# Kernel tuning notes

Hardware: AMD Instinct MI355X
Metric: run time of the kernel (lower is better)

The kernel has to match this reference:

```python
import jax, jax.numpy as jnp
import numpy as np

B, C, BINS, W, FF, NB = 8, 16, 1024, 512, 2048, 4
EPS = 1e-5
DN = ('NCH', 'OIH', 'NCH')  # conv1d dimension numbers


def setup_inputs() -> dict:
    key = jax.random.key(0)
    ks = iter(jax.random.split(key, 40))
    def w(shape, fan_in):
        return jax.random.normal(next(ks), shape, jnp.float32) / np.float32(np.sqrt(fan_in))
    inp = {}
    inp['x'] = jax.random.normal(next(ks), (B, C, BINS, W), jnp.float32)
    inp['bl_w'] = w((C, 1), C)                     # bottleneck linear
    inp['bn_w'] = jnp.ones((1,), jnp.float32)
    inp['bn_b'] = jnp.zeros((1,), jnp.float32)
    inp['glu_w'] = w((BINS, 2 * BINS), BINS)
    inp['ln1_w'] = jnp.ones((BINS,), jnp.float32); inp['ln1_b'] = jnp.zeros((BINS,), jnp.float32)
    inp['c1L_w'] = w((BINS, 2 * FF), BINS)
    inp['c1R_w'] = w((FF // 2, BINS, 3), BINS * 3)  # OIW conv weight
    inp['ln2_w'] = jnp.ones((2 * FF,), jnp.float32); inp['ln2_b'] = jnp.zeros((2 * FF,), jnp.float32)
    inp['c2d_w'] = w((2 * FF, 1, 9), 9)             # depthwise conv, groups=2*FF
    inp['c2p_w'] = w((FF // 2, 2 * FF, 1), 2 * FF)  # pointwise conv
    inp['ln3_w'] = jnp.ones((BINS,), jnp.float32); inp['ln3_b'] = jnp.zeros((BINS,), jnp.float32)
    inp['q_w'] = w((BINS, BINS), BINS)
    inp['k_w'] = w((BINS, BINS), BINS)
    inp['v_w'] = w((BINS, BINS), BINS)
    inp['o_w'] = w((BINS, BINS), BINS)
    inp['er'] = w((BINS // NB, W), BINS // NB)      # relative-position embedding
    inp['dist_w'] = w((NB, W, 1), W)                # distance weight per band
    inp['ln4_w'] = jnp.ones((BINS,), jnp.float32); inp['ln4_b'] = jnp.zeros((BINS,), jnp.float32)
    inp['c3_w'] = w((BINS, 2 * FF), BINS)
    inp['c4_w'] = w((2 * FF, BINS), 2 * FF)
    inp['ln5_w'] = jnp.ones((BINS,), jnp.float32); inp['ln5_b'] = jnp.zeros((BINS,), jnp.float32)
    return inp


def _ln(x, w, b):
    m = jnp.mean(x, -1, keepdims=True)
    v = jnp.mean((x - m) ** 2, -1, keepdims=True)
    return (x - m) * jax.lax.rsqrt(v + EPS) * w + b


def _forward(x, bl_w, bn_w, bn_b, glu_w, ln1_w, ln1_b, c1L_w, c1R_w, ln2_w, ln2_b,
             c2d_w, c2p_w, ln3_w, ln3_b, q_w, k_w, v_w, o_w, er, dist_w,
             ln4_w, ln4_b, c3_w, c4_w, ln5_w, ln5_b):
    # bottleneck: channels -> 1, BatchNorm2d (training-mode batch stats), ReLU
    y = jnp.einsum('bchw,co->bohw', x, bl_w)          # [B,1,BINS,W]
    m = jnp.mean(y, axis=(0, 2, 3), keepdims=True)
    v = jnp.mean((y - m) ** 2, axis=(0, 2, 3), keepdims=True)
    y = jax.nn.relu((y - m) * jax.lax.rsqrt(v + EPS) * bn_w.reshape(1, -1, 1, 1)
                    + bn_b.reshape(1, -1, 1, 1))
    xt = y[:, 0].transpose(0, 2, 1)                   # [B,W,BINS]

    # GLU branch + residual + LN
    g = xt @ glu_w
    a_, b_ = jnp.split(g, 2, axis=-1)
    xt = _ln(xt + a_ * jax.nn.sigmoid(b_), ln1_w, ln1_b)

    # dual branch: linear (wide) + conv1d (narrow, zero-padded up)
    hL = jax.nn.relu(xt @ c1L_w)                      # [B,W,2*FF]
    hR = jax.lax.conv_general_dilated(xt.transpose(0, 2, 1), c1R_w, (1,), ((1, 1),),
                                      dimension_numbers=DN).transpose(0, 2, 1)
    hR = jax.nn.relu(hR)                              # [B,W,FF//2]
    h = _ln(hL + jnp.pad(hR, ((0, 0), (0, 0), (0, 2 * FF - FF // 2))), ln2_w, ln2_b)

    # depthwise conv (k=9) + pointwise conv
    hc = jax.lax.conv_general_dilated(h.transpose(0, 2, 1), c2d_w, (1,), ((4, 4),),
                                      dimension_numbers=DN, feature_group_count=2 * FF)
    hc = jax.lax.conv_general_dilated(hc, c2p_w, (1,), ((0, 0),), dimension_numbers=DN)
    h = hc.transpose(0, 2, 1)                         # [B,W,FF//2]
    xt = _ln(xt + jnp.pad(h, ((0, 0), (0, 0), (0, BINS - FF // 2))), ln3_w, ln3_b)

    # multiband frame attention with relative-position bias
    d = BINS // NB
    q = (xt @ q_w).reshape(B, W, NB, d).transpose(0, 2, 1, 3)   # [B,NB,W,d]
    k = (xt @ k_w).reshape(B, W, NB, d).transpose(0, 2, 1, 3)
    vv = (xt @ v_w).reshape(B, W, NB, d).transpose(0, 2, 1, 3)
    qk = jnp.einsum('bnid,bnjd->bnij', q, k) / np.float32(np.sqrt(BINS))
    qe = jnp.einsum('bnid,dj->bnij', q, er)                      # [B,NB,W,W]
    skew = jnp.pad(qe, ((0, 0), (0, 0), (0, 0), (1, 0))).swapaxes(2, 3)[:, :, 1:, :]
    idx = jnp.arange(W)
    dist = jnp.abs(idx[:, None] - idx[None, :]).astype(jnp.float32) / 2.0  # [W,W]
    p = dist[None] * dist_w + skew                               # [B,NB,W,W]
    a = jax.nn.softmax(qk + p, axis=-1)
    o = jnp.einsum('bnij,bnjd->bnid', a, vv).transpose(0, 2, 1, 3).reshape(B, W, BINS) @ o_w
    xt = _ln(xt + o, ln4_w, ln4_b)

    # FFN
    h = jax.nn.relu(xt @ c3_w) @ c4_w
    xt = _ln(xt + h, ln5_w, ln5_b)
    return xt.transpose(0, 2, 1)[:, None]             # [B,1,BINS,W]


def reference(x, bl_w, bn_w, bn_b, glu_w, ln1_w, ln1_b, c1L_w, c1R_w, ln2_w, ln2_b,
              c2d_w, c2p_w, ln3_w, ln3_b, q_w, k_w, v_w, o_w, er, dist_w,
              ln4_w, ln4_b, c3_w, c4_w, ln5_w, ln5_b):
    return _forward(x, bl_w, bn_w, bn_b, glu_w, ln1_w, ln1_b, c1L_w, c1R_w, ln2_w, ln2_b,
                    c2d_w, c2p_w, ln3_w, ln3_b, q_w, k_w, v_w, o_w, er, dist_w,
                    ln4_w, ln4_b, c3_w, c4_w, ln5_w, ln5_b)
```

## Files before the change

kernel.cpp:

```cpp
#include <hip/hip_runtime.h>
#include <stdint.h>

typedef unsigned short u16;
typedef __bf16 bf16x8_t __attribute__((ext_vector_type(8)));
typedef float f32x4_t __attribute__((ext_vector_type(4)));
typedef u16 u16x8 __attribute__((ext_vector_type(8)));

#define DEVINL static __device__ __forceinline__

DEVINL float b2f(u16 h){ union{unsigned u; float f;} v; v.u=((unsigned)h)<<16; return v.f; }
DEVINL u16 f2b(float f){ union{float f; unsigned u;} v; v.f=f; unsigned u=v.u; u += 0x7fffu + ((u>>16)&1u); return (u16)(u>>16); }

DEVINL void gload16(const void* g, void* lds){
  __builtin_amdgcn_global_load_lds((__attribute__((address_space(1))) void*)(void*)g,
                                   (__attribute__((address_space(3))) void*)lds, 16, 0, 0);
}

DEVINL void blk_sum2(float& a, float& b, float* sm){
  #pragma unroll
  for (int o=32;o;o>>=1){ a += __shfl_down(a,o,64); b += __shfl_down(b,o,64); }
  int tid = threadIdx.x;
  if ((tid&63)==0){ sm[(tid>>6)*2]=a; sm[(tid>>6)*2+1]=b; }
  __syncthreads();
  a = sm[0]+sm[2]+sm[4]+sm[6];
  b = sm[1]+sm[3]+sm[5]+sm[7];
  __syncthreads();
}

template<int EPI>
__global__ __launch_bounds__(256) void gemm_k(
    const u16* __restrict__ A, int lda, long aS1, long aS2,
    const u16* __restrict__ B, int ldb, long bS1, long bS2,
    void* __restrict__ Cv, int ldc, long cS1, long cS2,
    int K, int zdiv)
{
  __shared__ u16 sA[128*32];
  __shared__ u16 sB[128*32];
  const int tid = threadIdx.x;
  const int w = tid >> 6, l = tid & 63;
  const int z = blockIdx.z; const int z1 = z / zdiv, z2 = z % zdiv;
  const u16* Ab = A + z1*aS1 + z2*aS2;
  const u16* Bb = B + z1*bS1 + z2*bS2;
  const int rowB = blockIdx.y * 128, colB = blockIdx.x * 128;

  const int sr = w*32 + (l>>2);
  const int so = (l&3)*8;
  const u16* gA0 = Ab + (long)(rowB + sr)*lda + so;
  const u16* gA1 = gA0 + (long)16*lda;
  const u16* gB0 = Bb + (long)(colB + sr)*ldb + so;
  const u16* gB1 = gB0 + (long)16*ldb;
  u16* lA0 = sA + w*1024; u16* lA1 = lA0 + 512;
  u16* lB0 = sB + w*1024; u16* lB1 = lB0 + 512;

  const int lrow = l & 15, lg = l >> 4;
  const int wrow = w & 1, wcol = w >> 1;

  f32x4_t zz = {0.f,0.f,0.f,0.f};
  f32x4_t acc[4][4];
  #pragma unroll
  for (int mi=0; mi<4; ++mi)
    #pragma unroll
    for (int ni=0; ni<4; ++ni) acc[mi][ni] = zz;

  for (int k0 = 0; k0 < K; k0 += 32) {
    __syncthreads();
    gload16(gA0 + k0, lA0);
    gload16(gA1 + k0, lA1);
    gload16(gB0 + k0, lB0);
    gload16(gB1 + k0, lB1);
    __syncthreads();
    bf16x8_t af[4], bfr[4];
    #pragma unroll
    for (int mi=0; mi<4; ++mi)
      af[mi] = *(const bf16x8_t*)&sA[(wrow*64 + mi*16 + lrow)*32 + lg*8];
    #pragma unroll
    for (int ni=0; ni<4; ++ni)
      bfr[ni] = *(const bf16x8_t*)&sB[(wcol*64 + ni*16 + lrow)*32 + lg*8];
    #pragma unroll
    for (int mi=0; mi<4; ++mi)
      #pragma unroll
      for (int ni=0; ni<4; ++ni)
        acc[mi][ni] = __builtin_amdgcn_mfma_f32_16x16x32_bf16(af[mi], bfr[ni], acc[mi][ni], 0,0,0);
  }

  const long cb = z1*cS1 + z2*cS2;
  #pragma unroll
  for (int mi=0; mi<4; ++mi)
  #pragma unroll
  for (int ni=0; ni<4; ++ni)
  #pragma unroll
  for (int j=0; j<4; ++j) {
    const long rr = rowB + wrow*64 + mi*16 + lg*4 + j;
    const long cc = colB + wcol*64 + ni*16 + lrow;
    float v = acc[mi][ni][j];
    if (EPI == 2) ((float*)Cv)[cb + rr*(long)ldc + cc] = v;
    else {
      if (EPI == 1) v = fmaxf(v, 0.f);
      ((u16*)Cv)[cb + rr*(long)ldc + cc] = f2b(v);
    }
  }
}

__global__ __launch_bounds__(256) void k_tcvt(const float* __restrict__ src, u16* __restrict__ dst, int R, int Cc){
  __shared__ float s[32][33];
  int c0 = blockIdx.x*32, r0 = blockIdx.y*32;
  int tx = threadIdx.x, ty = threadIdx.y;
  #pragma unroll
  for (int k=0;k<4;++k)
    s[ty+8*k][tx] = src[(long)(r0+ty+8*k)*Cc + c0+tx];
  __syncthreads();
  #pragma unroll
  for (int k=0;k<4;++k)
    dst[(long)(c0+ty+8*k)*R + r0+tx] = f2b(s[tx][ty+8*k]);
}

__global__ __launch_bounds__(256) void k_cvt(const float* __restrict__ src, u16* __restrict__ dst){
  long base = (long)blockIdx.x*1024 + threadIdx.x;
  #pragma unroll
  for (int j=0;j<4;++j) dst[base + j*256] = f2b(src[base + j*256]);
}

__global__ __launch_bounds__(256) void k_c1rp(const float* __restrict__ src, u16* __restrict__ dst){
  int o = blockIdx.x; int kk = blockIdx.y*256 + threadIdx.x;
  int i = kk & 1023, t = kk >> 10;
  dst[(long)o*3072 + kk] = f2b(src[(long)o*3072 + i*3 + t]);
}

__global__ __launch_bounds__(256) void k_cdt(const float* __restrict__ src, float* __restrict__ dst){
  int idx = blockIdx.x*256 + threadIdx.x;
  int t = idx >> 12, f = idx & 4095;
  dst[idx] = src[f*9 + t];
}

__global__ void k_zero(float* p){ if (threadIdx.x < 2) p[threadIdx.x] = 0.f; }

__global__ __launch_bounds__(256) void k_bneck1(const float* __restrict__ x, const float* __restrict__ blw,
                                                float* __restrict__ X, float* __restrict__ stats){
  __shared__ float s[64][65];
  __shared__ float red[8];
  int b = blockIdx.z, h0 = blockIdx.y*64, w0 = blockIdx.x*64;
  int tid = threadIdx.x;
  int wl = tid & 63, hl = tid >> 6;
  float yacc[16];
  #pragma unroll
  for (int r=0;r<16;++r) yacc[r]=0.f;
  for (int c=0;c<16;++c){
    float wc = blw[c];
    const float* xp = x + (((long)(b*16 + c)*1024 + h0)*512 + w0);
    #pragma unroll
    for (int r=0;r<16;++r)
      yacc[r] += xp[(hl + 4*r)*512 + wl] * wc;
  }
  float s1=0.f, s2=0.f;
  #pragma unroll
  for (int r=0;r<16;++r){ s1+=yacc[r]; s2+=yacc[r]*yacc[r]; }
  #pragma unroll
  for (int o=32;o;o>>=1){ s1+=__shfl_down(s1,o,64); s2+=__shfl_down(s2,o,64); }
  if ((tid&63)==0){ red[(tid>>6)*2]=s1; red[(tid>>6)*2+1]=s2; }
  #pragma unroll
  for (int r=0;r<16;++r) s[hl+4*r][wl] = yacc[r];
  __syncthreads();
  if (tid==0){
    atomicAdd(&stats[0], red[0]+red[2]+red[4]+red[6]);
    atomicAdd(&stats[1], red[1]+red[3]+red[5]+red[7]);
  }
  #pragma unroll
  for (int r=0;r<16;++r)
    X[((long)(b*512) + w0 + hl + 4*r)*1024 + h0 + wl] = s[wl][hl+4*r];
}

__global__ __launch_bounds__(256) void k_bneck2(float* __restrict__ X, u16* __restrict__ Xb,
                                                const float* __restrict__ stats,
                                                const float* __restrict__ bnw, const float* __restrict__ bnb){
  long base = (long)blockIdx.x*1024 + threadIdx.x;
  float mean = stats[0] * (1.f/4194304.f);
  float var  = stats[1] * (1.f/4194304.f) - mean*mean;
  float inv  = 1.f/sqrtf(var + 1e-5f);
  float w = bnw[0], bb = bnb[0];
  #pragma unroll
  for (int j=0;j<4;++j){
    float v = X[base + j*256];
    v = fmaxf((v - mean)*inv*w + bb, 0.f);
    X[base + j*256] = v; Xb[base + j*256] = f2b(v);
  }
}

__global__ __launch_bounds__(256) void k_glu_ln(const u16* __restrict__ g, float* __restrict__ X, u16* __restrict__ Xb,
                                                const float* __restrict__ lw, const float* __restrict__ lb){
  __shared__ float sm[8];
  long r = blockIdx.x; int tid = threadIdx.x;
  float u[4]; float s1=0.f, s2=0.f;
  #pragma unroll
  for (int j=0;j<4;++j){
    int i = j*256 + tid;
    float xv = X[r*1024 + i];
    float av = b2f(g[r*2048 + i]);
    float bv = b2f(g[r*2048 + 1024 + i]);
    float t = xv + av * (1.f/(1.f + expf(-bv)));
    u[j]=t; s1+=t; s2+=t*t;
  }
  blk_sum2(s1,s2,sm);
  float m = s1*(1.f/1024.f), var = s2*(1.f/1024.f)-m*m;
  float inv = 1.f/sqrtf(var+1e-5f);
  #pragma unroll
  for (int j=0;j<4;++j){
    int i=j*256+tid;
    float o = (u[j]-m)*inv*lw[i]+lb[i];
    X[r*1024+i]=o; Xb[r*1024+i]=f2b(o);
  }
}

__global__ __launch_bounds__(256) void k_res_ln(float* __restrict__ X, const u16* __restrict__ T, u16* __restrict__ Xb,
                                                const float* __restrict__ lw, const float* __restrict__ lb){
  __shared__ float sm[8];
  long r = blockIdx.x; int tid = threadIdx.x;
  float u[4]; float s1=0.f, s2=0.f;
  #pragma unroll
  for (int j=0;j<4;++j){
    int i = j*256 + tid;
    float t = X[r*1024 + i] + b2f(T[r*1024 + i]);
    u[j]=t; s1+=t; s2+=t*t;
  }
  blk_sum2(s1,s2,sm);
  float m = s1*(1.f/1024.f), var = s2*(1.f/1024.f)-m*m;
  float inv = 1.f/sqrtf(var+1e-5f);
  #pragma unroll
  for (int j=0;j<4;++j){
    int i=j*256+tid;
    float o = (u[j]-m)*inv*lw[i]+lb[i];
    X[r*1024+i]=o; Xb[r*1024+i]=f2b(o);
  }
}

__global__ __launch_bounds__(256) void k_add_ln4096(const u16* __restrict__ hL, const u16* __restrict__ hR,
                                                    u16* __restrict__ H,
                                                    const float* __restrict__ lw, const float* __restrict__ lb){
  __shared__ float sm[8];
  long r = blockIdx.x; int tid = threadIdx.x;
  float u[16]; float s1=0.f, s2=0.f;
  #pragma unroll
  for (int j=0;j<16;++j){
    int i = j*256 + tid;
    float t = b2f(hL[r*4096 + i]);
    if (j < 4) t += b2f(hR[r*1024 + i]);
    u[j]=t; s1+=t; s2+=t*t;
  }
  blk_sum2(s1,s2,sm);
  float m = s1*(1.f/4096.f), var = s2*(1.f/4096.f)-m*m;
  float inv = 1.f/sqrtf(var+1e-5f);
  #pragma unroll
  for (int j=0;j<16;++j){
    int i=j*256+tid;
    H[r*4096+i] = f2b((u[j]-m)*inv*lw[i]+lb[i]);
  }
}

__global__ __launch_bounds__(256) void k_gather(const u16* __restrict__ Xb, u16* __restrict__ Ab){
  int r = blockIdx.x;
  int b = r >> 9, wp = r & 511;
  for (int c = threadIdx.x; c < 384; c += 256){
    int t = c >> 7;
    int i0 = (c & 127) * 8;
    int ws_ = wp + t - 1;
    u16x8 v = {0,0,0,0,0,0,0,0};
    if (ws_ >= 0 && ws_ < 512) v = *(const u16x8*)&Xb[((long)(b*512+ws_))*1024 + i0];
    *(u16x8*)&Ab[(long)r*3072 + t*1024 + i0] = v;
  }
}

__global__ __launch_bounds__(256) void k_dw(const u16* __restrict__ H, const float* __restrict__ cdT,
                                            u16* __restrict__ HC){
  int r = blockIdx.y;
  int f0 = (blockIdx.x*256 + threadIdx.x)*8;
  int b = r>>9, wp = r&511;
  float acc[8] = {0.f,0.f,0.f,0.f,0.f,0.f,0.f,0.f};
  #pragma unroll
  for (int t=0;t<9;++t){
    int ww = wp + t - 4;
    if (ww < 0 || ww >= 512) continue;
    u16x8 hv = *(const u16x8*)&H[((long)(b*512+ww))*4096 + f0];
    f32x4_t c0 = *(const f32x4_t*)&cdT[t*4096 + f0];
    f32x4_t c1 = *(const f32x4_t*)&cdT[t*4096 + f0 + 4];
    acc[0] += b2f(hv[0]) * c0[0];
    acc[1] += b2f(hv[1]) * c0[1];
    acc[2] += b2f(hv[2]) * c0[2];
    acc[3] += b2f(hv[3]) * c0[3];
    acc[4] += b2f(hv[4]) * c1[0];
    acc[5] += b2f(hv[5]) * c1[1];
    acc[6] += b2f(hv[6]) * c1[2];
    acc[7] += b2f(hv[7]) * c1[3];
  }
  u16x8 o;
  #pragma unroll
  for (int e=0;e<8;++e) o[e] = f2b(acc[e]);
  *(u16x8*)&HC[(long)r*4096 + f0] = o;
}

__global__ __launch_bounds__(256) void k_tv(const u16* __restrict__ V, u16* __restrict__ VT){
  __shared__ u16 s[32][33];
  int z = blockIdx.z; int b = z>>2, n = z&3;
  int d0 = blockIdx.x*32, i0 = blockIdx.y*32;
  int tx = threadIdx.x, ty = threadIdx.y;
  const u16* src = V + (long)(b*512)*1024 + n*256;
  #pragma unroll
  for (int k=0;k<4;++k)
    s[ty+8*k][tx] = src[(long)(i0+ty+8*k)*1024 + d0 + tx];
  __syncthreads();
  u16* dst = VT + (long)z*131072;
  #pragma unroll
  for (int k=0;k<4;++k)
    dst[(long)(d0+ty+8*k)*512 + i0 + tx] = s[tx][ty+8*k];
}

__global__ __launch_bounds__(256) void k_softmax(const float* __restrict__ S, const u16* __restrict__ Et,
                                                 const float* __restrict__ dw, u16* __restrict__ P){
  __shared__ float sm[8];
  int id = blockIdx.x;
  int i = id & 511, n = (id>>9)&3;
  long base = (long)id * 512;
  float dwv = dw[n*512 + i];
  int tid = threadIdx.x;
  float sv[2]; float mx = -1e30f;
  #pragma unroll
  for (int j2=0;j2<2;++j2){
    int j = j2*256 + tid;
    float t = S[base+j]*0.03125f + fabsf((float)(i-j))*0.5f*dwv + b2f(Et[base+j]);
    sv[j2]=t; mx = fmaxf(mx,t);
  }
  #pragma unroll
  for (int o=32;o;o>>=1) mx = fmaxf(mx, __shfl_down(mx,o,64));
  if ((tid&63)==0) sm[tid>>6]=mx;
  __syncthreads();
  mx = fmaxf(fmaxf(sm[0],sm[1]),fmaxf(sm[2],sm[3]));
  __syncthreads();
  float ev[2]; float s1=0.f;
  #pragma unroll
  for (int j2=0;j2<2;++j2){ ev[j2]=expf(sv[j2]-mx); s1+=ev[j2]; }
  #pragma unroll
  for (int o=32;o;o>>=1) s1 += __shfl_down(s1,o,64);
  if ((tid&63)==0) sm[tid>>6]=s1;
  __syncthreads();
  s1 = sm[0]+sm[1]+sm[2]+sm[3];
  float rr = 1.f/s1;
  #pragma unroll
  for (int j2=0;j2<2;++j2) P[base + j2*256 + tid] = f2b(ev[j2]*rr);
}

__global__ __launch_bounds__(256) void k_final(const float* __restrict__ X, float* __restrict__ out){
  __shared__ float s[64][65];
  int b = blockIdx.z, h0 = blockIdx.y*64, w0 = blockIdx.x*64;
  int tid = threadIdx.x;
  int a = tid & 63, q = tid >> 6;
  #pragma unroll
  for (int r=0;r<16;++r)
    s[q+4*r][a] = X[((long)(b*512)+w0+q+4*r)*1024 + h0 + a];
  __syncthreads();
  #pragma unroll
  for (int r=0;r<16;++r)
    out[((long)(b*1024)+h0+q+4*r)*512 + w0 + a] = s[a][q+4*r];
}

extern "C" void kernel_launch(void* const* d_in, const int* in_sizes, int n_in,
                              void* d_out, int out_size, void* d_ws, size_t ws_size,
                              hipStream_t stream) {
  const float* x      = (const float*)d_in[0];
  const float* bl_w   = (const float*)d_in[1];
  const float* bn_w   = (const float*)d_in[2];
  const float* bn_b   = (const float*)d_in[3];
  const float* glu_w  = (const float*)d_in[4];
  const float* ln1_w  = (const float*)d_in[5];
  const float* ln1_b  = (const float*)d_in[6];
  const float* c1L_w  = (const float*)d_in[7];
  const float* c1R_w  = (const float*)d_in[8];
  const float* ln2_w  = (const float*)d_in[9];
  const float* ln2_b  = (const float*)d_in[10];
  const float* c2d_w  = (const float*)d_in[11];
  const float* c2p_w  = (const float*)d_in[12];
  const float* ln3_w  = (const float*)d_in[13];
  const float* ln3_b  = (const float*)d_in[14];
  const float* q_w    = (const float*)d_in[15];
  const float* k_w    = (const float*)d_in[16];
  const float* v_w    = (const float*)d_in[17];
  const float* o_w    = (const float*)d_in[18];
  const float* er     = (const float*)d_in[19];
  const float* dist_w = (const float*)d_in[20];
  const float* ln4_w  = (const float*)d_in[21];
  const float* ln4_b  = (const float*)d_in[22];
  const float* c3_w   = (const float*)d_in[23];
  const float* c4_w   = (const float*)d_in[24];
  const float* ln5_w  = (const float*)d_in[25];
  const float* ln5_b  = (const float*)d_in[26];

  char* ws = (char*)d_ws;
  size_t off = 0;
  auto alloc = [&](size_t n){ size_t o = off; off = (off + n + 255) & ~(size_t)255; return o; };

  size_t o_wglu = alloc(2048ull*1024*2);
  size_t o_wc1L = alloc(4096ull*1024*2);
  size_t o_wc1R = alloc(1024ull*3072*2);
  size_t o_wc2p = alloc(1024ull*4096*2);
  size_t o_wq   = alloc(1024ull*1024*2);
  size_t o_wk   = alloc(1024ull*1024*2);
  size_t o_wv   = alloc(1024ull*1024*2);
  size_t o_wo   = alloc(1024ull*1024*2);
  size_t o_wert = alloc(512ull*256*2);
  size_t o_wc3  = alloc(4096ull*1024*2);
  size_t o_wc4  = alloc(1024ull*4096*2);
  size_t o_cdt  = alloc(9ull*4096*4);
  size_t o_X    = alloc(4096ull*1024*4);
  size_t o_Xb   = alloc(4096ull*1024*2);
  size_t o_A1   = alloc(33554432);
  size_t o_A2   = alloc(33554432);
  size_t o_A3   = alloc(33554432);
  size_t o_A4   = alloc(16777216);
  size_t o_st   = alloc(256);
  (void)ws_size; (void)n_in; (void)in_sizes; (void)out_size;

  u16* WGLU = (u16*)(ws+o_wglu); u16* WC1L = (u16*)(ws+o_wc1L); u16* WC1R = (u16*)(ws+o_wc1R);
  u16* WC2P = (u16*)(ws+o_wc2p); u16* WQ = (u16*)(ws+o_wq); u16* WK = (u16*)(ws+o_wk);
  u16* WV = (u16*)(ws+o_wv); u16* WO = (u16*)(ws+o_wo); u16* WERT = (u16*)(ws+o_wert);
  u16* WC3 = (u16*)(ws+o_wc3); u16* WC4 = (u16*)(ws+o_wc4);
  float* CDT = (float*)(ws+o_cdt);
  float* X = (float*)(ws+o_X); u16* Xb = (u16*)(ws+o_Xb);
  u16* A1 = (u16*)(ws+o_A1); u16* A2 = (u16*)(ws+o_A2);
  u16* A3 = (u16*)(ws+o_A3); u16* A4 = (u16*)(ws+o_A4);
  float* stats = (float*)(ws+o_st);

  auto GEMM = [&](int epi, const u16* A, int lda, long aS1, long aS2,
                  const u16* B, int ldb, long bS1, long bS2,
                  void* C, int ldc, long cS1, long cS2,
                  int M, int N, int K, int zdiv, int nz){
    dim3 grid(N/128, M/128, nz);
    if (epi==0)      gemm_k<0><<<grid,256,0,stream>>>(A,lda,aS1,aS2,B,ldb,bS1,bS2,C,ldc,cS1,cS2,K,zdiv);
    else if (epi==1) gemm_k<1><<<grid,256,0,stream>>>(A,lda,aS1,aS2,B,ldb,bS1,bS2,C,ldc,cS1,cS2,K,zdiv);
    else             gemm_k<2><<<grid,256,0,stream>>>(A,lda,aS1,aS2,B,ldb,bS1,bS2,C,ldc,cS1,cS2,K,zdiv);
  };

  k_zero<<<1,64,0,stream>>>(stats);
  k_tcvt<<<dim3(64,32),dim3(32,8),0,stream>>>(glu_w, WGLU, 1024, 2048);
  k_tcvt<<<dim3(128,32),dim3(32,8),0,stream>>>(c1L_w, WC1L, 1024, 4096);
  k_c1rp<<<dim3(1024,12),256,0,stream>>>(c1R_w, WC1R);
  k_cvt<<<4096,256,0,stream>>>(c2p_w, WC2P);
  k_cdt<<<144,256,0,stream>>>(c2d_w, CDT);
  k_tcvt<<<dim3(32,32),dim3(32,8),0,stream>>>(q_w, WQ, 1024, 1024);
  k_tcvt<<<dim3(32,32),dim3(32,8),0,stream>>>(k_w, WK, 1024, 1024);
  k_tcvt<<<dim3(32,32),dim3(32,8),0,stream>>>(v_w, WV, 1024, 1024);
  k_tcvt<<<dim3(32,32),dim3(32,8),0,stream>>>(o_w, WO, 1024, 1024);
  k_tcvt<<<dim3(16,8),dim3(32,8),0,stream>>>(er, WERT, 256, 512);
  k_tcvt<<<dim3(128,32),dim3(32,8),0,stream>>>(c3_w, WC3, 1024, 4096);
  k_tcvt<<<dim3(32,128),dim3(32,8),0,stream>>>(c4_w, WC4, 4096, 1024);

  k_bneck1<<<dim3(8,16,8),256,0,stream>>>(x, bl_w, X, stats);
  k_bneck2<<<4096,256,0,stream>>>(X, Xb, stats, bn_w, bn_b);

  GEMM(0, Xb,1024,0,0, WGLU,1024,0,0, A1,2048,0,0, 4096,2048,1024, 1,1);
  k_glu_ln<<<4096,256,0,stream>>>(A1, X, Xb, ln1_w, ln1_b);

  k_gather<<<4096,256,0,stream>>>(Xb, A3);
  GEMM(1, Xb,1024,0,0, WC1L,1024,0,0, A1,4096,0,0, 4096,4096,1024, 1,1);
  GEMM(1, A3,3072,0,0, WC1R,3072,0,0, A4,1024,0,0, 4096,1024,3072, 1,1);
  k_add_ln4096<<<4096,256,0,stream>>>(A1, A4, A2, ln2_w, ln2_b);

  k_dw<<<dim3(2,4096),256,0,stream>>>(A2, CDT, A1);
  GEMM(0, A1,4096,0,0, WC2P,4096,0,0, A4,1024,0,0, 4096,1024,4096, 1,1);
  k_res_ln<<<4096,256,0,stream>>>(X, A4, Xb, ln3_w, ln3_b);

  u16* Aq = A1;
  u16* Ak = A1 + 4194304;
  u16* Av = A1 + 8388608;
  GEMM(0, Xb,1024,0,0, WQ,1024,0,0, Aq,1024,0,0, 4096,1024,1024, 1,1);
  GEMM(0, Xb,1024,0,0, WK,1024,0,0, Ak,1024,0,0, 4096,1024,1024, 1,1);
  GEMM(0, Xb,1024,0,0, WV,1024,0,0, Av,1024,0,0, 4096,1024,1024, 1,1);
  u16* VT = A2;
  k_tv<<<dim3(8,16,32),dim3(32,8),0,stream>>>(Av, VT);
  float* Sf = (float*)A3;
  GEMM(2, Aq,1024,524288,256, Ak,1024,524288,256, Sf,512,1048576,262144, 512,512,256, 4,32);
  u16* EtB = (u16*)(ws + o_A2 + 8388608);
  GEMM(0, WERT,256,0,0, Aq,1024,524288,256, EtB,512,1048576,262144, 512,512,256, 4,32);
  u16* P = A4;
  k_softmax<<<16384,256,0,stream>>>(Sf, EtB, dist_w, P);
  u16* Ov = A1;
  GEMM(0, P,512,1048576,262144, VT,512,524288,131072, Ov,1024,524288,256, 512,256,512, 4,32);
  u16* AOp = A3;
  GEMM(0, Ov,1024,0,0, WO,1024,0,0, AOp,1024,0,0, 4096,1024,1024, 1,1);
  k_res_ln<<<4096,256,0,stream>>>(X, AOp, Xb, ln4_w, ln4_b);

  GEMM(1, Xb,1024,0,0, WC3,1024,0,0, A1,4096,0,0, 4096,4096,1024, 1,1);
  GEMM(0, A1,4096,0,0, WC4,4096,0,0, A4,1024,0,0, 4096,1024,4096, 1,1);
  k_res_ln<<<4096,256,0,stream>>>(X, A4, Xb, ln5_w, ln5_b);

  k_final<<<dim3(8,16,8),256,0,stream>>>(X, (float*)d_out);
}
```

Baseline: 1.302 ms.

## Split-K narrow GEMMs, fuse QKV projection, and remap workgroups across XCDs

The N=1024 GEMMs (c1R, c2p, o-proj, c4) are now split into two K halves. Each half writes fp32 partials, and the following LayerNorm kernels add the two partials, applying ReLU for the c1R path. The three Q/K/V projections are merged into one GEMM with a concatenated 3072-wide weight, and downstream strides are adjusted to match. The GEMM kernel also remaps block IDs so consecutive tiles land on the same XCD for better L2 locality. These changes raise the block count for under-filled grids and cut launches, at the cost of extra fp32 partial traffic and a new 32MB workspace buffer.

```diff
diff --git a/kernel.cpp b/kernel.cpp
--- a/kernel.cpp
+++ b/kernel.cpp
@@ -41,7 +41,14 @@
   const int z = blockIdx.z; const int z1 = z / zdiv, z2 = z % zdiv;
   const u16* Ab = A + z1*aS1 + z2*aS2;
   const u16* Bb = B + z1*bS1 + z2*bS2;
-  const int rowB = blockIdx.y * 128, colB = blockIdx.x * 128;
+
+  const int gx = gridDim.x;
+  const int nwg = gx * gridDim.y;
+  const int orig = blockIdx.y*gx + blockIdx.x;
+  const int qq = nwg >> 3, rr8 = nwg & 7;
+  const int xcd = orig & 7, idx8 = orig >> 3;
+  const int wgid = (xcd < rr8 ? xcd*(qq+1) : rr8*(qq+1) + (xcd-rr8)*qq) + idx8;
+  const int rowB = (wgid / gx) * 128, colB = (wgid % gx) * 128;
 
   const int sr = w*32 + (l>>2);
   const int so = (l&3)*8;
@@ -210,15 +217,15 @@
   }
 }
 
-__global__ __launch_bounds__(256) void k_res_ln(float* __restrict__ X, const u16* __restrict__ T, u16* __restrict__ Xb,
-                                                const float* __restrict__ lw, const float* __restrict__ lb){
+__global__ __launch_bounds__(256) void k_res_ln2(float* __restrict__ X, const float* __restrict__ P, u16* __restrict__ Xb,
+                                                 const float* __restrict__ lw, const float* __restrict__ lb){
   __shared__ float sm[8];
   long r = blockIdx.x; int tid = threadIdx.x;
   float u[4]; float s1=0.f, s2=0.f;
   #pragma unroll
   for (int j=0;j<4;++j){
     int i = j*256 + tid;
-    float t = X[r*1024 + i] + b2f(T[r*1024 + i]);
+    float t = X[r*1024 + i] + P[r*1024 + i] + P[4194304 + r*1024 + i];
     u[j]=t; s1+=t; s2+=t*t;
   }
   blk_sum2(s1,s2,sm);
@@ -232,9 +239,9 @@
   }
 }
 
-__global__ __launch_bounds__(256) void k_add_ln4096(const u16* __restrict__ hL, const u16* __restrict__ hR,
-                                                    u16* __restrict__ H,
-                                                    const float* __restrict__ lw, const float* __restrict__ lb){
+__global__ __launch_bounds__(256) void k_add_ln4096_2(const u16* __restrict__ hL, const float* __restrict__ P,
+                                                      u16* __restrict__ H,
+                                                      const float* __restrict__ lw, const float* __restrict__ lb){
   __shared__ float sm[8];
   long r = blockIdx.x; int tid = threadIdx.x;
   float u[16]; float s1=0.f, s2=0.f;
@@ -242,7 +249,7 @@
   for (int j=0;j<16;++j){
     int i = j*256 + tid;
     float t = b2f(hL[r*4096 + i]);
-    if (j < 4) t += b2f(hR[r*1024 + i]);
+    if (j < 4) t += fmaxf(P[r*1024 + i] + P[4194304 + r*1024 + i], 0.f);
     u[j]=t; s1+=t; s2+=t*t;
   }
   blk_sum2(s1,s2,sm);
@@ -296,15 +303,15 @@
   *(u16x8*)&HC[(long)r*4096 + f0] = o;
 }
 
-__global__ __launch_bounds__(256) void k_tv(const u16* __restrict__ V, u16* __restrict__ VT){
+__global__ __launch_bounds__(256) void k_tv(const u16* __restrict__ V, u16* __restrict__ VT, int lda){
   __shared__ u16 s[32][33];
   int z = blockIdx.z; int b = z>>2, n = z&3;
   int d0 = blockIdx.x*32, i0 = blockIdx.y*32;
   int tx = threadIdx.x, ty = threadIdx.y;
-  const u16* src = V + (long)(b*512)*1024 + n*256;
+  const u16* src = V + (long)(b*512)*lda + n*256;
   #pragma unroll
   for (int k=0;k<4;++k)
-    s[ty+8*k][tx] = src[(long)(i0+ty+8*k)*1024 + d0 + tx];
+    s[ty+8*k][tx] = src[(long)(i0+ty+8*k)*lda + d0 + tx];
   __syncthreads();
   u16* dst = VT + (long)z*131072;
   #pragma unroll
@@ -399,9 +406,7 @@
   size_t o_wc1L = alloc(4096ull*1024*2);
   size_t o_wc1R = alloc(1024ull*3072*2);
   size_t o_wc2p = alloc(1024ull*4096*2);
-  size_t o_wq   = alloc(1024ull*1024*2);
-  size_t o_wk   = alloc(1024ull*1024*2);
-  size_t o_wv   = alloc(1024ull*1024*2);
+  size_t o_wqkv = alloc(3072ull*1024*2);
   size_t o_wo   = alloc(1024ull*1024*2);
   size_t o_wert = alloc(512ull*256*2);
   size_t o_wc3  = alloc(4096ull*1024*2);
@@ -413,17 +418,19 @@
   size_t o_A2   = alloc(33554432);
   size_t o_A3   = alloc(33554432);
   size_t o_A4   = alloc(16777216);
+  size_t o_A5   = alloc(33554432);
   size_t o_st   = alloc(256);
   (void)ws_size; (void)n_in; (void)in_sizes; (void)out_size;
 
   u16* WGLU = (u16*)(ws+o_wglu); u16* WC1L = (u16*)(ws+o_wc1L); u16* WC1R = (u16*)(ws+o_wc1R);
-  u16* WC2P = (u16*)(ws+o_wc2p); u16* WQ = (u16*)(ws+o_wq); u16* WK = (u16*)(ws+o_wk);
-  u16* WV = (u16*)(ws+o_wv); u16* WO = (u16*)(ws+o_wo); u16* WERT = (u16*)(ws+o_wert);
+  u16* WC2P = (u16*)(ws+o_wc2p); u16* WQKV = (u16*)(ws+o_wqkv);
+  u16* WO = (u16*)(ws+o_wo); u16* WERT = (u16*)(ws+o_wert);
   u16* WC3 = (u16*)(ws+o_wc3); u16* WC4 = (u16*)(ws+o_wc4);
   float* CDT = (float*)(ws+o_cdt);
   float* X = (float*)(ws+o_X); u16* Xb = (u16*)(ws+o_Xb);
   u16* A1 = (u16*)(ws+o_A1); u16* A2 = (u16*)(ws+o_A2);
   u16* A3 = (u16*)(ws+o_A3); u16* A4 = (u16*)(ws+o_A4);
+  float* A5 = (float*)(ws+o_A5);
   float* stats = (float*)(ws+o_st);
 
   auto GEMM = [&](int epi, const u16* A, int lda, long aS1, long aS2,
@@ -442,9 +449,9 @@
   k_c1rp<<<dim3(1024,12),256,0,stream>>>(c1R_w, WC1R);
   k_cvt<<<4096,256,0,stream>>>(c2p_w, WC2P);
   k_cdt<<<144,256,0,stream>>>(c2d_w, CDT);
-  k_tcvt<<<dim3(32,32),dim3(32,8),0,stream>>>(q_w, WQ, 1024, 1024);
-  k_tcvt<<<dim3(32,32),dim3(32,8),0,stream>>>(k_w, WK, 1024, 1024);
-  k_tcvt<<<dim3(32,32),dim3(32,8),0,stream>>>(v_w, WV, 1024, 1024);
+  k_tcvt<<<dim3(32,32),dim3(32,8),0,stream>>>(q_w, WQKV, 1024, 1024);
+  k_tcvt<<<dim3(32,32),dim3(32,8),0,stream>>>(k_w, WQKV + 1048576, 1024, 1024);
+  k_tcvt<<<dim3(32,32),dim3(32,8),0,stream>>>(v_w, WQKV + 2097152, 1024, 1024);
   k_tcvt<<<dim3(32,32),dim3(32,8),0,stream>>>(o_w, WO, 1024, 1024);
   k_tcvt<<<dim3(16,8),dim3(32,8),0,stream>>>(er, WERT, 256, 512);
   k_tcvt<<<dim3(128,32),dim3(32,8),0,stream>>>(c3_w, WC3, 1024, 4096);
@@ -458,36 +465,34 @@
 
   k_gather<<<4096,256,0,stream>>>(Xb, A3);
   GEMM(1, Xb,1024,0,0, WC1L,1024,0,0, A1,4096,0,0, 4096,4096,1024, 1,1);
-  GEMM(1, A3,3072,0,0, WC1R,3072,0,0, A4,1024,0,0, 4096,1024,3072, 1,1);
-  k_add_ln4096<<<4096,256,0,stream>>>(A1, A4, A2, ln2_w, ln2_b);
+  GEMM(2, A3,3072,1536,0, WC1R,3072,1536,0, A5,1024,4194304,0, 4096,1024,1536, 1,2);
+  k_add_ln4096_2<<<4096,256,0,stream>>>(A1, A5, A2, ln2_w, ln2_b);
 
   k_dw<<<dim3(2,4096),256,0,stream>>>(A2, CDT, A1);
-  GEMM(0, A1,4096,0,0, WC2P,4096,0,0, A4,1024,0,0, 4096,1024,4096, 1,1);
-  k_res_ln<<<4096,256,0,stream>>>(X, A4, Xb, ln3_w, ln3_b);
-
-  u16* Aq = A1;
-  u16* Ak = A1 + 4194304;
-  u16* Av = A1 + 8388608;
-  GEMM(0, Xb,1024,0,0, WQ,1024,0,0, Aq,1024,0,0, 4096,1024,1024, 1,1);
-  GEMM(0, Xb,1024,0,0, WK,1024,0,0, Ak,1024,0,0, 4096,1024,1024, 1,1);
-  GEMM(0, Xb,1024,0,0, WV,1024,0,0, Av,1024,0,0, 4096,1024,1024, 1,1);
+  GEMM(2, A1,4096,2048,0, WC2P,4096,2048,0, A5,1024,4194304,0, 4096,1024,2048, 1,2);
+  k_res_ln2<<<4096,256,0,stream>>>(X, A5, Xb, ln3_w, ln3_b);
+
+  u16* AQKV = A1;
+  GEMM(0, Xb,1024,0,0, WQKV,1024,0,0, AQKV,3072,0,0, 4096,3072,1024, 1,1);
+  const u16* Aq = AQKV;
+  const u16* Ak = AQKV + 1024;
+  const u16* Av = AQKV + 2048;
   u16* VT = A2;
-  k_tv<<<dim3(8,16,32),dim3(32,8),0,stream>>>(Av, VT);
+  k_tv<<<dim3(8,16,32),dim3(32,8),0,stream>>>(Av, VT, 3072);
   float* Sf = (float*)A3;
-  GEMM(2, Aq,1024,524288,256, Ak,1024,524288,256, Sf,512,1048576,262144, 512,512,256, 4,32);
+  GEMM(2, Aq,3072,1572864,256, Ak,3072,1572864,256, Sf,512,1048576,262144, 512,512,256, 4,32);
   u16* EtB = (u16*)(ws + o_A2 + 8388608);
-  GEMM(0, WERT,256,0,0, Aq,1024,524288,256, EtB,512,1048576,262144, 512,512,256, 4,32);
+  GEMM(0, WERT,256,0,0, Aq,3072,1572864,256, EtB,512,1048576,262144, 512,512,256, 4,32);
   u16* P = A4;
   k_softmax<<<16384,256,0,stream>>>(Sf, EtB, dist_w, P);
   u16* Ov = A1;
   GEMM(0, P,512,1048576,262144, VT,512,524288,131072, Ov,1024,524288,256, 512,256,512, 4,32);
-  u16* AOp = A3;
-  GEMM(0, Ov,1024,0,0, WO,1024,0,0, AOp,1024,0,0, 4096,1024,1024, 1,1);
-  k_res_ln<<<4096,256,0,stream>>>(X, AOp, Xb, ln4_w, ln4_b);
+  GEMM(2, Ov,1024,512,0, WO,1024,512,0, A5,1024,4194304,0, 4096,1024,512, 1,2);
+  k_res_ln2<<<4096,256,0,stream>>>(X, A5, Xb, ln4_w, ln4_b);
 
   GEMM(1, Xb,1024,0,0, WC3,1024,0,0, A1,4096,0,0, 4096,4096,1024, 1,1);
-  GEMM(0, A1,4096,0,0, WC4,4096,0,0, A4,1024,0,0, 4096,1024,4096, 1,1);
-  k_res_ln<<<4096,256,0,stream>>>(X, A4, Xb, ln5_w, ln5_b);
+  GEMM(2, A1,4096,2048,0, WC4,4096,2048,0, A5,1024,4194304,0, 4096,1024,2048, 1,2);
+  k_res_ln2<<<4096,256,0,stream>>>(X, A5, Xb, ln5_w, ln5_b);
 
   k_final<<<dim3(8,16,8),256,0,stream>>>(X, (float*)d_out);
 }
```

Result: faster. 1.102 ms (-15.3%).
